# Optimization experiments

Measured on AMD Instinct MI355X. Metric: run time of the kernel, lower is better.

Reference implementation:

```python
import jax, jax.numpy as jnp
import numpy as np

N = 50000        # nodes
E = 800000       # edges (before self-loops)
NFEAT = 256
NHID = 32
HEADS = 8
NOUT = 128
NEG_SLOPE = 0.2
EPS = 1e-5


def _gat_layer(x, src, dst, W, att_src, att_dst, bias, heads, ch, concat):
    """PyG-style GATConv (shared weights for src/dst, self-loops already appended)."""
    n = x.shape[0]
    h = (x @ W).reshape(n, heads, ch)                      # [N,H,C]
    a_src = (h * att_src).sum(-1)                          # [N,H]
    a_dst = (h * att_dst).sum(-1)                          # [N,H]
    e = jax.nn.leaky_relu(a_src[src] + a_dst[dst], NEG_SLOPE)  # [E',H]
    # segment softmax over incoming edges of each dst node
    m = jax.ops.segment_max(e, dst, num_segments=n)        # [N,H]
    m = jnp.where(jnp.isfinite(m), m, 0.0)
    ex = jnp.exp(e - m[dst])                               # [E',H]
    denom = jax.ops.segment_sum(ex, dst, num_segments=n)   # [N,H]
    alpha = ex / (denom[dst] + 1e-16)                      # [E',H]
    msg = h[src] * alpha[:, :, None]                       # [E',H,C]
    out = jax.ops.segment_sum(msg, dst, num_segments=n)    # [N,H,C]
    out = out.reshape(n, heads * ch) if concat else out.mean(axis=1)
    return out + bias


def setup_inputs() -> dict:
    key = jax.random.key(0)
    ks = jax.random.split(key, 14)
    s = 0.05
    return {
        "x": jax.random.normal(ks[0], (N, NFEAT), jnp.float32),
        "edge_index": jax.random.randint(ks[1], (2, E), 0, N, dtype=jnp.int64),
        "W1": jax.random.normal(ks[2], (NFEAT, HEADS * NHID), jnp.float32) * s,
        "att_src1": jax.random.normal(ks[3], (HEADS, NHID), jnp.float32) * s,
        "att_dst1": jax.random.normal(ks[4], (HEADS, NHID), jnp.float32) * s,
        "b1": jnp.zeros((HEADS * NHID,), jnp.float32),
        "W2": jax.random.normal(ks[5], (HEADS * NHID, NOUT), jnp.float32) * s,
        "att_src2": jax.random.normal(ks[6], (1, NOUT), jnp.float32) * s,
        "att_dst2": jax.random.normal(ks[7], (1, NOUT), jnp.float32) * s,
        "b2": jnp.zeros((NOUT,), jnp.float32),
        "bn_gamma": jnp.ones((NOUT,), jnp.float32),
        "bn_beta": jnp.zeros((NOUT,), jnp.float32),
        "ln_gamma": jnp.ones((NOUT,), jnp.float32),
        "ln_beta": jnp.zeros((NOUT,), jnp.float32),
    }


def reference(x, edge_index, W1, att_src1, att_dst1, b1, W2, att_src2, att_dst2, b2,
              bn_gamma, bn_beta, ln_gamma, ln_beta):
    loops = jnp.arange(N, dtype=edge_index.dtype)
    src = jnp.concatenate([edge_index[0], loops])
    dst = jnp.concatenate([edge_index[1], loops])
    # layer 1: concat heads, then relu (dropout is identity at inference)
    h = jax.nn.relu(_gat_layer(x, src, dst, W1, att_src1, att_dst1, b1, HEADS, NHID, True))
    # layer 2: single head, mean (no concat), relu
    h = jax.nn.relu(_gat_layer(h, src, dst, W2, att_src2, att_dst2, b2, 1, NOUT, False))
    # BatchNorm1d with batch statistics (biased var, eps=1e-5)
    mu = h.mean(axis=0)
    var = h.var(axis=0)
    h = (h - mu) / jnp.sqrt(var + EPS) * bn_gamma + bn_beta
    # LayerNorm over last dim
    mu2 = h.mean(axis=-1, keepdims=True)
    var2 = h.var(axis=-1, keepdims=True)
    return (h - mu2) / jnp.sqrt(var2 + EPS) * ln_gamma + ln_beta
```

## Files before the change

kernel.cpp:

```cpp
#include <hip/hip_runtime.h>
#include <cstdint>
#include <cstddef>

#define HEADS   8
#define NFEAT   256
#define NOUT    128
#define NEG     0.2f
#define EPSV    1e-5f

typedef unsigned short ushort_t;
typedef __attribute__((ext_vector_type(8))) short s8v;
typedef __attribute__((ext_vector_type(4))) float f4v;

static __device__ __forceinline__ float lrelu(float x) { return x > 0.f ? x : NEG * x; }

static __device__ __forceinline__ float bf2f(ushort_t u) {
    union { unsigned int i; float f; } v; v.i = ((unsigned int)u) << 16; return v.f;
}
static __device__ __forceinline__ ushort_t f2bf(float f) {
    union { float f; unsigned int i; } v; v.f = f;
    unsigned int x = v.i;
    return (ushort_t)((x + 0x7fff + ((x >> 16) & 1)) >> 16);
}
static __device__ __forceinline__ float bits2f(unsigned int u) {
    union { unsigned int i; float f; } v; v.i = u; return v.f;
}
static __device__ __forceinline__ unsigned int f2bits(float f) {
    union { float f; unsigned int i; } v; v.f = f; return v.i;
}

static __device__ __forceinline__ int detect64(const int* __restrict__ ei, int E) {
    int lane = threadIdx.x & 63;
    long idx = 2L * ((long)lane * (E / 64)) + 1;
    int v = ei[idx];
    unsigned long long ball = __ballot(v == 0);
    return (ball == ~0ull) ? 1 : 0;
}

__global__ void k_prep(const int* __restrict__ ei, int* __restrict__ counts,
                       int E, int n, int cblocks,
                       const float* __restrict__ W1, const float* __restrict__ W2,
                       ushort_t* __restrict__ Wh1, ushort_t* __restrict__ Wl1,
                       ushort_t* __restrict__ Wh2, ushort_t* __restrict__ Wl2) {
    if (blockIdx.x < (unsigned)cblocks) {
        int is64 = detect64(ei, E);
        int i = blockIdx.x * 256 + threadIdx.x;
        if (i < E) {
            int d = ei[(size_t)(E + i) << is64];
            atomicAdd(&counts[d], 1);
        } else if (i < E + n) {
            atomicAdd(&counts[i - E], 1);
        }
    } else {
        int gid = (blockIdx.x - cblocks) * 256 + threadIdx.x;
        const float* W; ushort_t* Wh; ushort_t* Wl; int M;
        if (gid < 256 * 256) { W = W1; Wh = Wh1; Wl = Wl1; M = 256; }
        else { gid -= 256 * 256; if (gid >= 256 * 128) return; W = W2; Wh = Wh2; Wl = Wl2; M = 128; }
        int k = gid / M, nn = gid - k * M;
        int ntile = nn >> 4, j = nn & 15, kc = k >> 3, e = k & 7;
        int p = ((ntile * 32 + kc) * 16 + j) * 8 + e;
        float v = W[(size_t)k * M + nn];
        ushort_t hi = f2bf(v);
        float r = v - bf2f(hi);
        Wh[p] = hi;
        Wl[p] = f2bf(r);
    }
}

__global__ __launch_bounds__(1024) void k_scan1(const int* __restrict__ counts,
                                                int* __restrict__ incl,
                                                int* __restrict__ bsum, int n) {
    int t = threadIdx.x, i = blockIdx.x * 1024 + t;
    int lane = t & 63, w = t >> 6;
    int v = (i < n) ? counts[i] : 0;
    int sv = v;
#pragma unroll
    for (int o = 1; o < 64; o <<= 1) { int u = __shfl_up(sv, o, 64); if (lane >= o) sv += u; }
    __shared__ int wsum[16];
    if (lane == 63) wsum[w] = sv;
    __syncthreads();
    if (w == 0) {
        int bs = (lane < 16) ? wsum[lane] : 0;
#pragma unroll
        for (int o = 1; o < 16; o <<= 1) { int u = __shfl_up(bs, o, 64); if (lane >= o) bs += u; }
        if (lane < 16) wsum[lane] = bs;
    }
    __syncthreads();
    int pre = (w > 0) ? wsum[w - 1] : 0;
    sv += pre;
    if (i < n) incl[i] = sv;
    if (t == 1023) bsum[blockIdx.x] = sv;
}

__global__ void k_scan3(const int* __restrict__ incl, const int* __restrict__ bsum,
                        const int* __restrict__ counts,
                        int* __restrict__ offs, int* __restrict__ cursor, int n) {
    __shared__ int pre_s;
    int chunk = blockIdx.x >> 2;
    if (threadIdx.x == 0) {
        int s = 0;
        for (int j = 0; j < chunk; ++j) s += bsum[j];
        pre_s = s;
    }
    __syncthreads();
    int i = blockIdx.x * 256 + threadIdx.x;
    if (i < n) {
        int v = incl[i] + pre_s;
        offs[i + 1] = v;
        cursor[i] = v - counts[i];
    }
    if (i == 0) offs[0] = 0;
}

__global__ void k_fill(const int* __restrict__ ei, int* __restrict__ cursor,
                       int* __restrict__ esrc, int E, int n) {
    int is64 = detect64(ei, E);
    int i = blockIdx.x * blockDim.x + threadIdx.x;
    if (i >= E + n) return;
    int s, d;
    if (i < E) { s = ei[(size_t)i << is64]; d = ei[(size_t)(E + i) << is64]; }
    else       { s = i - E; d = s; }
    int p = atomicAdd(&cursor[d], 1);
    esrc[p] = s;
}

template <int MOUT>
__global__ __launch_bounds__(256) void k_mm(const float* __restrict__ A,
                                            const ushort_t* __restrict__ Wh,
                                            const ushort_t* __restrict__ Wl,
                                            ushort_t* __restrict__ C,
                                            const float* __restrict__ att_s,
                                            const float* __restrict__ att_d,
                                            float* __restrict__ as_o,
                                            float* __restrict__ ad_o, int n) {
    __shared__ ushort_t Ah[64][40];
    __shared__ ushort_t Al[64][40];
    const int t = threadIdx.x;
    const int lane = t & 63, w = t >> 6;
    const int r0 = blockIdx.x * 64;
    const int srow = t >> 2;
    const int kh = (t & 3) * 8;
    const int arow = r0 + srow;
    const bool rowok = arow < n;

    f4v acc[4][2];
#pragma unroll
    for (int a = 0; a < 4; ++a)
#pragma unroll
        for (int b = 0; b < 2; ++b) { f4v z = {0.f, 0.f, 0.f, 0.f}; acc[a][b] = z; }

    float pre[8];
    const float* abase = &A[(size_t)arow * 256 + kh];
#pragma unroll
    for (int q = 0; q < 2; ++q) {
        float4 v = rowok ? *reinterpret_cast<const float4*>(abase + q * 4)
                         : float4{0.f, 0.f, 0.f, 0.f};
        pre[q * 4 + 0] = v.x; pre[q * 4 + 1] = v.y;
        pre[q * 4 + 2] = v.z; pre[q * 4 + 3] = v.w;
    }

    const int lj = lane & 15, lk = lane >> 4;

    for (int kb = 0; kb < 256; kb += 32) {
        __syncthreads();
        {
            unsigned int hw[4], lw[4];
#pragma unroll
            for (int p = 0; p < 4; ++p) {
                unsigned int x0 = f2bits(pre[p * 2]);
                unsigned int x1 = f2bits(pre[p * 2 + 1]);
                unsigned int h1b = x1 & 0xffff0000u;
                float lo0 = pre[p * 2] - bits2f(x0 & 0xffff0000u);
                float lo1 = pre[p * 2 + 1] - bits2f(h1b);
                hw[p] = (x0 >> 16) | h1b;
                lw[p] = (f2bits(lo0) >> 16) | (f2bits(lo1) & 0xffff0000u);
            }
            uint4 hv = {hw[0], hw[1], hw[2], hw[3]};
            uint4 lv = {lw[0], lw[1], lw[2], lw[3]};
            *reinterpret_cast<uint4*>(&Ah[srow][kh]) = hv;
            *reinterpret_cast<uint4*>(&Al[srow][kh]) = lv;
        }
        __syncthreads();
        if (kb < 224) {
            const float* ap = abase + kb + 32;
#pragma unroll
            for (int q = 0; q < 2; ++q) {
                float4 v = rowok ? *reinterpret_cast<const float4*>(ap + q * 4)
                                 : float4{0.f, 0.f, 0.f, 0.f};
                pre[q * 4 + 0] = v.x; pre[q * 4 + 1] = v.y;
                pre[q * 4 + 2] = v.z; pre[q * 4 + 3] = v.w;
            }
        }
        const int kc0 = kb >> 3;
        s8v ah[4], al[4];
#pragma unroll
        for (int mf = 0; mf < 4; ++mf) {
            ah[mf] = *reinterpret_cast<const s8v*>(&Ah[mf * 16 + lj][lk * 8]);
            al[mf] = *reinterpret_cast<const s8v*>(&Al[mf * 16 + lj][lk * 8]);
        }
#pragma unroll
        for (int nf = 0; nf < 2; ++nf) {
            int ntile = (MOUT == 256 ? blockIdx.y * 8 : 0) + w * 2 + nf;
            size_t boff = ((size_t)(ntile * 32 + kc0 + lk) * 16 + lj) * 8;
            s8v bh = *reinterpret_cast<const s8v*>(&Wh[boff]);
            s8v bl = *reinterpret_cast<const s8v*>(&Wl[boff]);
#pragma unroll
            for (int mf = 0; mf < 4; ++mf) {
                acc[mf][nf] = __builtin_amdgcn_mfma_f32_16x16x32_bf16(ah[mf], bh, acc[mf][nf], 0, 0, 0);
                acc[mf][nf] = __builtin_amdgcn_mfma_f32_16x16x32_bf16(ah[mf], bl, acc[mf][nf], 0, 0, 0);
                acc[mf][nf] = __builtin_amdgcn_mfma_f32_16x16x32_bf16(al[mf], bh, acc[mf][nf], 0, 0, 0);
            }
        }
    }

    const int colw = (MOUT == 256 ? blockIdx.y * 128 : 0) + w * 32;

#pragma unroll
    for (int mf = 0; mf < 4; ++mf) {
        int rr = r0 + mf * 16 + lk * 4;
#pragma unroll
        for (int nf = 0; nf < 2; ++nf) {
            int cc = colw + nf * 16 + lj;
#pragma unroll
            for (int r = 0; r < 4; ++r) {
                if (rr + r < n) C[(size_t)(rr + r) * MOUT + cc] = f2bf(acc[mf][nf][r]);
            }
        }
    }

    float asv[2], adv[2];
#pragma unroll
    for (int nf = 0; nf < 2; ++nf) {
        asv[nf] = att_s[colw + nf * 16 + lj];
        adv[nf] = att_d[colw + nf * 16 + lj];
    }
#pragma unroll
    for (int mf = 0; mf < 4; ++mf) {
        int rr = r0 + mf * 16 + lk * 4;
#pragma unroll
        for (int r = 0; r < 4; ++r) {
            float ss = acc[mf][0][r] * asv[0] + acc[mf][1][r] * asv[1];
            float sd = acc[mf][0][r] * adv[0] + acc[mf][1][r] * adv[1];
#pragma unroll
            for (int o = 1; o < 16; o <<= 1) {
                ss += __shfl_xor(ss, o, 64); sd += __shfl_xor(sd, o, 64);
            }
            if (lj == 0 && rr + r < n) {
                if (MOUT == 256) {
                    int head = (colw >> 5);
                    as_o[(size_t)(rr + r) * 8 + head] = ss;
                    ad_o[(size_t)(rr + r) * 8 + head] = sd;
                } else {
                    atomicAdd(&as_o[rr + r], ss);
                    atomicAdd(&ad_o[rr + r], sd);
                }
            }
        }
    }
}

__global__ __launch_bounds__(128) void k_agg1(const ushort_t* __restrict__ h1,
                                              const float* __restrict__ as1,
                                              const float* __restrict__ ad1,
                                              const int* __restrict__ offs,
                                              const int* __restrict__ esrc,
                                              const float* __restrict__ b1,
                                              float* __restrict__ out1, int n, int tot) {
    int wid = (blockIdx.x * 128 + threadIdx.x) >> 6;
    int lane = threadIdx.x & 63;
    if (wid >= n) return;
    int e0 = offs[wid], e1 = offs[wid + 1];
    int deg = e1 - e0;

    if (deg <= 64) {
        const int l = lane & 31;
        const int h = lane >> 5;
        const int hd = l >> 2;
        const int cb = l * 8;

        int ei_idx = e0 + lane;
        int es = esrc[ei_idx < tot ? ei_idx : (tot - 1)];

        const int headA = lane >> 3, g = lane & 7;
        float adnA = ad1[(size_t)wid * 8 + headA];
        float a[8];
#pragma unroll
        for (int k = 0; k < 8; ++k) {
            int i = g + 8 * k;
            int s = __shfl(es, i, 64);
            a[k] = (i < deg) ? as1[(size_t)s * 8 + headA] : -1e30f;
        }
        float mx = a[0];
#pragma unroll
        for (int k = 1; k < 8; ++k) mx = fmaxf(mx, a[k]);
#pragma unroll
        for (int o = 1; o < 8; o <<= 1) mx = fmaxf(mx, __shfl_xor(mx, o, 64));
        float mA = lrelu(mx + adnA);
#pragma unroll
        for (int k = 0; k < 8; ++k)
            a[k] = __expf(lrelu(a[k] + adnA) - mA);

        float d = 0.f;
        float ac0 = 0.f, ac1 = 0.f, ac2 = 0.f, ac3 = 0.f;
        float ac4 = 0.f, ac5 = 0.f, ac6 = 0.f, ac7 = 0.f;
#pragma unroll
        for (int u = 0; u < 8; ++u) {
            if (8 * u < deg) {
#pragma unroll
                for (int v = 0; v < 4; ++v) {
                    int i = 8 * u + 2 * v + h;
                    int s = __shfl(es, i, 64);
                    float p = __shfl(a[u], hd * 8 + 2 * v + h, 64);
                    if (i < deg) {
                        uint4 hv = *reinterpret_cast<const uint4*>(&h1[(size_t)s * 256 + cb]);
                        d += p;
                        ac0 += p * bits2f(hv.x << 16);
                        ac1 += p * bits2f(hv.x & 0xffff0000u);
                        ac2 += p * bits2f(hv.y << 16);
                        ac3 += p * bits2f(hv.y & 0xffff0000u);
                        ac4 += p * bits2f(hv.z << 16);
                        ac5 += p * bits2f(hv.z & 0xffff0000u);
                        ac6 += p * bits2f(hv.w << 16);
                        ac7 += p * bits2f(hv.w & 0xffff0000u);
                    }
                }
            }
        }
        d   += __shfl_xor(d, 32, 64);
        ac0 += __shfl_xor(ac0, 32, 64); ac1 += __shfl_xor(ac1, 32, 64);
        ac2 += __shfl_xor(ac2, 32, 64); ac3 += __shfl_xor(ac3, 32, 64);
        ac4 += __shfl_xor(ac4, 32, 64); ac5 += __shfl_xor(ac5, 32, 64);
        ac6 += __shfl_xor(ac6, 32, 64); ac7 += __shfl_xor(ac7, 32, 64);
        if (lane < 32) {
            float inv = 1.f / (d + 1e-16f);
            float4 b0 = *reinterpret_cast<const float4*>(&b1[cb]);
            float4 b4 = *reinterpret_cast<const float4*>(&b1[cb + 4]);
            float4 o0, o1;
            o0.x = fmaxf(ac0 * inv + b0.x, 0.f);
            o0.y = fmaxf(ac1 * inv + b0.y, 0.f);
            o0.z = fmaxf(ac2 * inv + b0.z, 0.f);
            o0.w = fmaxf(ac3 * inv + b0.w, 0.f);
            o1.x = fmaxf(ac4 * inv + b4.x, 0.f);
            o1.y = fmaxf(ac5 * inv + b4.y, 0.f);
            o1.z = fmaxf(ac6 * inv + b4.z, 0.f);
            o1.w = fmaxf(ac7 * inv + b4.w, 0.f);
            *reinterpret_cast<float4*>(&out1[(size_t)wid * 256 + cb]) = o0;
            *reinterpret_cast<float4*>(&out1[(size_t)wid * 256 + cb + 4]) = o1;
        }
    } else {
        int head = lane >> 3;
        int g = lane & 7;
        int cb = lane * 4;
        float adn = ad1[(size_t)wid * 8 + head];
        float mx = -1e30f;
        for (int e = e0 + g; e < e1; e += 8)
            mx = fmaxf(mx, as1[(size_t)esrc[e] * 8 + head]);
#pragma unroll
        for (int o = 1; o < 8; o <<= 1) mx = fmaxf(mx, __shfl_xor(mx, o, 64));
        float m = lrelu(mx + adn);
        float d = 0.f, ax = 0.f, ay = 0.f, az = 0.f, aw = 0.f;
        for (int e = e0; e < e1; ++e) {
            int s = esrc[e];
            float p = __expf(lrelu(as1[(size_t)s * 8 + head] + adn) - m);
            ushort4 hv = *reinterpret_cast<const ushort4*>(&h1[(size_t)s * 256 + cb]);
            d += p;
            ax += p * bf2f(hv.x);
            ay += p * bf2f(hv.y);
            az += p * bf2f(hv.z);
            aw += p * bf2f(hv.w);
        }
        float inv = 1.f / (d + 1e-16f);
        float4 bb = *reinterpret_cast<const float4*>(&b1[cb]);
        float4 o;
        o.x = fmaxf(ax * inv + bb.x, 0.f);
        o.y = fmaxf(ay * inv + bb.y, 0.f);
        o.z = fmaxf(az * inv + bb.z, 0.f);
        o.w = fmaxf(aw * inv + bb.w, 0.f);
        *reinterpret_cast<float4*>(&out1[(size_t)wid * 256 + cb]) = o;
    }
}

__global__ __launch_bounds__(128) void k_agg2(const ushort_t* __restrict__ h2,
                                              const float* __restrict__ as2,
                                              const float* __restrict__ ad2,
                                              const int* __restrict__ offs,
                                              const int* __restrict__ esrc,
                                              const float* __restrict__ b2,
                                              float* __restrict__ out2, int n, int tot) {
    int wid = (blockIdx.x * 128 + threadIdx.x) >> 6;
    int lane = threadIdx.x & 63;
    if (wid >= n) return;
    float adn = ad2[wid];
    int e0 = offs[wid], e1 = offs[wid + 1];
    int deg = e1 - e0;

    if (deg <= 64) {
        const int l = lane & 15;
        const int q = lane >> 4;
        const int cb = l * 8;

        int ei_idx = e0 + lane;
        int es = esrc[ei_idx < tot ? ei_idx : (tot - 1)];
        float av0 = (lane < deg) ? as2[es] : -1e30f;
        float mx = av0;
#pragma unroll
        for (int o = 1; o < 64; o <<= 1) mx = fmaxf(mx, __shfl_xor(mx, o, 64));
        float m = lrelu(mx + adn);
        float p0 = __expf(lrelu(av0 + adn) - m);

        float d = 0.f;
        float ac0 = 0.f, ac1 = 0.f, ac2 = 0.f, ac3 = 0.f;
        float ac4 = 0.f, ac5 = 0.f, ac6 = 0.f, ac7 = 0.f;
#pragma unroll
        for (int u = 0; u < 4; ++u) {
            if (16 * u < deg) {
#pragma unroll
                for (int v = 0; v < 4; ++v) {
                    int i = 16 * u + 4 * v + q;
                    int s = __shfl(es, i, 64);
                    float p = __shfl(p0, i, 64);
                    if (i < deg) {
                        uint4 hv = *reinterpret_cast<const uint4*>(&h2[(size_t)s * 128 + cb]);
                        d += p;
                        ac0 += p * bits2f(hv.x << 16);
                        ac1 += p * bits2f(hv.x & 0xffff0000u);
                        ac2 += p * bits2f(hv.y << 16);
                        ac3 += p * bits2f(hv.y & 0xffff0000u);
                        ac4 += p * bits2f(hv.z << 16);
                        ac5 += p * bits2f(hv.z & 0xffff0000u);
                        ac6 += p * bits2f(hv.w << 16);
                        ac7 += p * bits2f(hv.w & 0xffff0000u);
                    }
                }
            }
        }
#pragma unroll
        for (int o = 16; o <= 32; o <<= 1) {
            d   += __shfl_xor(d, o, 64);
            ac0 += __shfl_xor(ac0, o, 64); ac1 += __shfl_xor(ac1, o, 64);
            ac2 += __shfl_xor(ac2, o, 64); ac3 += __shfl_xor(ac3, o, 64);
            ac4 += __shfl_xor(ac4, o, 64); ac5 += __shfl_xor(ac5, o, 64);
            ac6 += __shfl_xor(ac6, o, 64); ac7 += __shfl_xor(ac7, o, 64);
        }
        if (lane < 16) {
            float inv = 1.f / (d + 1e-16f);
            float4 b0 = *reinterpret_cast<const float4*>(&b2[cb]);
            float4 b4 = *reinterpret_cast<const float4*>(&b2[cb + 4]);
            float4 o0, o1;
            o0.x = fmaxf(ac0 * inv + b0.x, 0.f);
            o0.y = fmaxf(ac1 * inv + b0.y, 0.f);
            o0.z = fmaxf(ac2 * inv + b0.z, 0.f);
            o0.w = fmaxf(ac3 * inv + b0.w, 0.f);
            o1.x = fmaxf(ac4 * inv + b4.x, 0.f);
            o1.y = fmaxf(ac5 * inv + b4.y, 0.f);
            o1.z = fmaxf(ac6 * inv + b4.z, 0.f);
            o1.w = fmaxf(ac7 * inv + b4.w, 0.f);
            *reinterpret_cast<float4*>(&out2[(size_t)wid * 128 + cb]) = o0;
            *reinterpret_cast<float4*>(&out2[(size_t)wid * 128 + cb + 4]) = o1;
        }
    } else {
        int cb = lane * 2;
        float mx = -1e30f;
        for (int e = e0 + lane; e < e1; e += 64)
            mx = fmaxf(mx, as2[esrc[e]]);
#pragma unroll
        for (int o = 1; o < 64; o <<= 1) mx = fmaxf(mx, __shfl_xor(mx, o, 64));
        float m = lrelu(mx + adn);
        float d = 0.f, ax = 0.f, ay = 0.f;
        for (int e = e0; e < e1; ++e) {
            int s = esrc[e];
            float p = __expf(lrelu(as2[s] + adn) - m);
            ushort2 hv = *reinterpret_cast<const ushort2*>(&h2[(size_t)s * 128 + cb]);
            d += p;
            ax += p * bf2f(hv.x);
            ay += p * bf2f(hv.y);
        }
        float inv = 1.f / (d + 1e-16f);
        float o0 = fmaxf(ax * inv + b2[cb], 0.f);
        float o1 = fmaxf(ay * inv + b2[cb + 1], 0.f);
        float2 o = {o0, o1};
        *reinterpret_cast<float2*>(&out2[(size_t)wid * 128 + cb]) = o;
    }
}

__global__ __launch_bounds__(128) void k_bnstat(const float* __restrict__ out2,
                                                float* __restrict__ bnsum,
                                                float* __restrict__ bnsq, int n) {
    int c = threadIdx.x;
    float s = 0.f, q = 0.f;
    for (int r = blockIdx.x; r < n; r += gridDim.x) {
        float v = out2[(size_t)r * 128 + c];
        s += v;
        q += v * v;
    }
    atomicAdd(&bnsum[c], s);
    atomicAdd(&bnsq[c], q);
}

__global__ __launch_bounds__(256) void k_final(const float* __restrict__ out2,
                                               const float* __restrict__ bnsum,
                                               const float* __restrict__ bnsq,
                                               const float* __restrict__ bng,
                                               const float* __restrict__ bnb,
                                               const float* __restrict__ lng,
                                               const float* __restrict__ lnb,
                                               float* __restrict__ out, int n) {
    int wid = (blockIdx.x * blockDim.x + threadIdx.x) >> 6;
    int lane = threadIdx.x & 63;
    if (wid >= n) return;
    int c0 = lane, c1 = lane + 64;
    float invn = 1.f / (float)n;
    float mu0 = bnsum[c0] * invn, mu1 = bnsum[c1] * invn;
    float v0 = bnsq[c0] * invn - mu0 * mu0;
    float v1 = bnsq[c1] * invn - mu1 * mu1;
    float r0 = rsqrtf(v0 + EPSV), r1 = rsqrtf(v1 + EPSV);
    float x0 = out2[(size_t)wid * 128 + c0];
    float x1 = out2[(size_t)wid * 128 + c1];
    float y0 = (x0 - mu0) * r0 * bng[c0] + bnb[c0];
    float y1 = (x1 - mu1) * r1 * bng[c1] + bnb[c1];
    float s = y0 + y1, q = y0 * y0 + y1 * y1;
#pragma unroll
    for (int o = 1; o < 64; o <<= 1) { s += __shfl_xor(s, o, 64); q += __shfl_xor(q, o, 64); }
    float mu = s * (1.f / 128.f);
    float var = q * (1.f / 128.f) - mu * mu;
    float rr = rsqrtf(var + EPSV);
    out[(size_t)wid * 128 + c0] = (y0 - mu) * rr * lng[c0] + lnb[c0];
    out[(size_t)wid * 128 + c1] = (y1 - mu) * rr * lng[c1] + lnb[c1];
}

extern "C" void kernel_launch(void* const* d_in, const int* in_sizes, int n_in,
                              void* d_out, int out_size, void* d_ws, size_t ws_size,
                              hipStream_t stream) {
    const float* x    = (const float*)d_in[0];
    const int*   ei   = (const int*)d_in[1];
    const float* W1   = (const float*)d_in[2];
    const float* ats1 = (const float*)d_in[3];
    const float* atd1 = (const float*)d_in[4];
    const float* b1   = (const float*)d_in[5];
    const float* W2   = (const float*)d_in[6];
    const float* ats2 = (const float*)d_in[7];
    const float* atd2 = (const float*)d_in[8];
    const float* b2   = (const float*)d_in[9];
    const float* bng  = (const float*)d_in[10];
    const float* bnb  = (const float*)d_in[11];
    const float* lng  = (const float*)d_in[12];
    const float* lnb  = (const float*)d_in[13];

    const int n = in_sizes[0] / NFEAT;
    const int E = in_sizes[1] / 2;
    const int tot = E + n;

    auto align = [](size_t v) { return (v + 255) & ~(size_t)255; };
    char* ws = (char*)d_ws;
    size_t off = 0;
    ushort_t* h1 = (ushort_t*)(ws + off); off += align((size_t)n * 256 * 2);
    float* out1 = (float*)(ws + off); off += align((size_t)n * 256 * 4);
    ushort_t* h2 = h1;
    float* out2 = out1;
    float* as1 = (float*)(ws + off); off += align((size_t)n * 8 * 4);
    float* ad1 = (float*)(ws + off); off += align((size_t)n * 8 * 4);
    int* counts = (int*)(ws + off); off += align((size_t)n * 12 + 1024);
    float* bnsum = (float*)(counts + n);
    float* bnsq  = bnsum + 128;
    float* as2   = bnsq + 128;
    float* ad2   = as2 + n;
    int* offs   = (int*)(ws + off); off += align((size_t)(n + 1) * 4);
    int* cursor = (int*)(ws + off); off += align((size_t)n * 4);
    int* esrc   = (int*)(ws + off); off += align((size_t)tot * 4);
    int* incl   = (int*)(ws + off); off += align((size_t)n * 4);
    int* bsum   = (int*)(ws + off); off += align(64 * 4);
    ushort_t* Wh1 = (ushort_t*)(ws + off); off += align((size_t)256 * 256 * 2);
    ushort_t* Wl1 = (ushort_t*)(ws + off); off += align((size_t)256 * 256 * 2);
    ushort_t* Wh2 = (ushort_t*)(ws + off); off += align((size_t)256 * 128 * 2);
    ushort_t* Wl2 = (ushort_t*)(ws + off); off += align((size_t)256 * 128 * 2);

    hipMemsetAsync(counts, 0, (size_t)n * 12 + 1024, stream);

    const int cblocks = (tot + 255) / 256;
    const int pblocks = (256 * 256 + 256 * 128 + 255) / 256;
    k_prep<<<cblocks + pblocks, 256, 0, stream>>>(ei, counts, E, n, cblocks,
                                                  W1, W2, Wh1, Wl1, Wh2, Wl2);
    int nsb = (n + 1023) / 1024;
    k_scan1<<<nsb, 1024, 0, stream>>>(counts, incl, bsum, n);
    k_scan3<<<(n + 255) / 256, 256, 0, stream>>>(incl, bsum, counts, offs, cursor, n);
    k_fill<<<(tot + 255) / 256, 256, 0, stream>>>(ei, cursor, esrc, E, n);

    const int gx = (n + 63) / 64;
    k_mm<256><<<dim3(gx, 2), 256, 0, stream>>>(x, Wh1, Wl1, h1, ats1, atd1, as1, ad1, n);
    k_agg1<<<(n + 1) / 2, 128, 0, stream>>>(h1, as1, ad1, offs, esrc, b1, out1, n, tot);

    k_mm<128><<<dim3(gx, 1), 256, 0, stream>>>(out1, Wh2, Wl2, h2, ats2, atd2, as2, ad2, n);
    k_agg2<<<(n + 1) / 2, 128, 0, stream>>>(h2, as2, ad2, offs, esrc, b2, out2, n, tot);

    k_bnstat<<<512, 128, 0, stream>>>(out2, bnsum, bnsq, n);
    k_final<<<(n + 3) / 4, 256, 0, stream>>>(out2, bnsum, bnsq, bng, bnb, lng, lnb,
                                             (float*)d_out, n);
}
```

Before: 339.9 us.

## Double-buffer matmul LDS tiles and software-prefetch gathers in aggregation kernels

```diff
diff --git a/kernel.cpp b/kernel.cpp
--- a/kernel.cpp
+++ b/kernel.cpp
@@ -27,6 +27,19 @@
 }
 static __device__ __forceinline__ unsigned int f2bits(float f) {
     union { float f; unsigned int i; } v; v.f = f; return v.i;
+}
+
+static __device__ __forceinline__ void fma8(float p, const uint4& hv,
+    float& a0, float& a1, float& a2, float& a3,
+    float& a4, float& a5, float& a6, float& a7) {
+    a0 += p * bits2f(hv.x << 16);
+    a1 += p * bits2f(hv.x & 0xffff0000u);
+    a2 += p * bits2f(hv.y << 16);
+    a3 += p * bits2f(hv.y & 0xffff0000u);
+    a4 += p * bits2f(hv.z << 16);
+    a5 += p * bits2f(hv.z & 0xffff0000u);
+    a6 += p * bits2f(hv.w << 16);
+    a7 += p * bits2f(hv.w & 0xffff0000u);
 }
 
 static __device__ __forceinline__ int detect64(const int* __restrict__ ei, int E) {
@@ -133,8 +146,8 @@
                                             const float* __restrict__ att_d,
                                             float* __restrict__ as_o,
                                             float* __restrict__ ad_o, int n) {
-    __shared__ ushort_t Ah[64][40];
-    __shared__ ushort_t Al[64][40];
+    __shared__ ushort_t Ah[2][64][40];
+    __shared__ ushort_t Al[2][64][40];
     const int t = threadIdx.x;
     const int lane = t & 63, w = t >> 6;
     const int r0 = blockIdx.x * 64;
@@ -142,6 +155,7 @@
     const int kh = (t & 3) * 8;
     const int arow = r0 + srow;
     const bool rowok = arow < n;
+    const int lj = lane & 15, lk = lane >> 4;
 
     f4v acc[4][2];
 #pragma unroll
@@ -149,8 +163,70 @@
 #pragma unroll
         for (int b = 0; b < 2; ++b) { f4v z = {0.f, 0.f, 0.f, 0.f}; acc[a][b] = z; }
 
+    const float* abase = &A[(size_t)arow * 256 + kh];
     float pre[8];
-    const float* abase = &A[(size_t)arow * 256 + kh];
+
+#define MM_STAGE(BUF)                                                         \
+    {                                                                         \
+        unsigned int hw[4], lw[4];                                            \
+        _Pragma("unroll")                                                     \
+        for (int p = 0; p < 4; ++p) {                                         \
+            unsigned int x0 = f2bits(pre[p * 2]);                             \
+            unsigned int x1 = f2bits(pre[p * 2 + 1]);                         \
+            unsigned int h1b = x1 & 0xffff0000u;                              \
+            float lo0 = pre[p * 2] - bits2f(x0 & 0xffff0000u);                \
+            float lo1 = pre[p * 2 + 1] - bits2f(h1b);                         \
+            hw[p] = (x0 >> 16) | h1b;                                         \
+            lw[p] = (f2bits(lo0) >> 16) | (f2bits(lo1) & 0xffff0000u);        \
+        }                                                                     \
+        uint4 hv = {hw[0], hw[1], hw[2], hw[3]};                              \
+        uint4 lv = {lw[0], lw[1], lw[2], lw[3]};                              \
+        *reinterpret_cast<uint4*>(&Ah[BUF][srow][kh]) = hv;                   \
+        *reinterpret_cast<uint4*>(&Al[BUF][srow][kh]) = lv;                   \
+    }
+
+#define MM_LOADB(KB, BH, BL)                                                  \
+    {                                                                         \
+        const int kc0_ = (KB) >> 3;                                           \
+        _Pragma("unroll")                                                     \
+        for (int nf = 0; nf < 2; ++nf) {                                      \
+            int ntile = (MOUT == 256 ? blockIdx.y * 8 : 0) + w * 2 + nf;      \
+            size_t boff = ((size_t)(ntile * 32 + kc0_ + lk) * 16 + lj) * 8;   \
+            BH[nf] = *reinterpret_cast<const s8v*>(&Wh[boff]);                \
+            BL[nf] = *reinterpret_cast<const s8v*>(&Wl[boff]);                \
+        }                                                                     \
+    }
+
+#define MM_STEP(KB, CUR, BH, BL, BHN, BLN)                                    \
+    {                                                                         \
+        if ((KB) < 224) {                                                     \
+            const float* ap = abase + (KB) + 32;                              \
+            _Pragma("unroll")                                                 \
+            for (int q = 0; q < 2; ++q) {                                     \
+                float4 v = rowok ? *reinterpret_cast<const float4*>(ap + q*4) \
+                                 : float4{0.f, 0.f, 0.f, 0.f};                \
+                pre[q*4+0]=v.x; pre[q*4+1]=v.y; pre[q*4+2]=v.z; pre[q*4+3]=v.w; \
+            }                                                                 \
+            MM_LOADB((KB) + 32, BHN, BLN);                                    \
+        }                                                                     \
+        s8v ah[4], al[4];                                                     \
+        _Pragma("unroll")                                                     \
+        for (int mf = 0; mf < 4; ++mf) {                                      \
+            ah[mf] = *reinterpret_cast<const s8v*>(&Ah[CUR][mf*16+lj][lk*8]); \
+            al[mf] = *reinterpret_cast<const s8v*>(&Al[CUR][mf*16+lj][lk*8]); \
+        }                                                                     \
+        _Pragma("unroll")                                                     \
+        for (int nf = 0; nf < 2; ++nf)                                        \
+            _Pragma("unroll")                                                 \
+            for (int mf = 0; mf < 4; ++mf) {                                  \
+                acc[mf][nf] = __builtin_amdgcn_mfma_f32_16x16x32_bf16(ah[mf], BH[nf], acc[mf][nf], 0, 0, 0); \
+                acc[mf][nf] = __builtin_amdgcn_mfma_f32_16x16x32_bf16(ah[mf], BL[nf], acc[mf][nf], 0, 0, 0); \
+                acc[mf][nf] = __builtin_amdgcn_mfma_f32_16x16x32_bf16(al[mf], BH[nf], acc[mf][nf], 0, 0, 0); \
+            }                                                                 \
+        if ((KB) < 224) MM_STAGE((CUR) ^ 1);                                  \
+        __syncthreads();                                                      \
+    }
+
 #pragma unroll
     for (int q = 0; q < 2; ++q) {
         float4 v = rowok ? *reinterpret_cast<const float4*>(abase + q * 4)
@@ -158,59 +234,14 @@
         pre[q * 4 + 0] = v.x; pre[q * 4 + 1] = v.y;
         pre[q * 4 + 2] = v.z; pre[q * 4 + 3] = v.w;
     }
-
-    const int lj = lane & 15, lk = lane >> 4;
-
-    for (int kb = 0; kb < 256; kb += 32) {
-        __syncthreads();
-        {
-            unsigned int hw[4], lw[4];
-#pragma unroll
-            for (int p = 0; p < 4; ++p) {
-                unsigned int x0 = f2bits(pre[p * 2]);
-                unsigned int x1 = f2bits(pre[p * 2 + 1]);
-                unsigned int h1b = x1 & 0xffff0000u;
-                float lo0 = pre[p * 2] - bits2f(x0 & 0xffff0000u);
-                float lo1 = pre[p * 2 + 1] - bits2f(h1b);
-                hw[p] = (x0 >> 16) | h1b;
-                lw[p] = (f2bits(lo0) >> 16) | (f2bits(lo1) & 0xffff0000u);
-            }
-            uint4 hv = {hw[0], hw[1], hw[2], hw[3]};
-            uint4 lv = {lw[0], lw[1], lw[2], lw[3]};
-            *reinterpret_cast<uint4*>(&Ah[srow][kh]) = hv;
-            *reinterpret_cast<uint4*>(&Al[srow][kh]) = lv;
-        }
-        __syncthreads();
-        if (kb < 224) {
-            const float* ap = abase + kb + 32;
-#pragma unroll
-            for (int q = 0; q < 2; ++q) {
-                float4 v = rowok ? *reinterpret_cast<const float4*>(ap + q * 4)
-                                 : float4{0.f, 0.f, 0.f, 0.f};
-                pre[q * 4 + 0] = v.x; pre[q * 4 + 1] = v.y;
-                pre[q * 4 + 2] = v.z; pre[q * 4 + 3] = v.w;
-            }
-        }
-        const int kc0 = kb >> 3;
-        s8v ah[4], al[4];
-#pragma unroll
-        for (int mf = 0; mf < 4; ++mf) {
-            ah[mf] = *reinterpret_cast<const s8v*>(&Ah[mf * 16 + lj][lk * 8]);
-            al[mf] = *reinterpret_cast<const s8v*>(&Al[mf * 16 + lj][lk * 8]);
-        }
-#pragma unroll
-        for (int nf = 0; nf < 2; ++nf) {
-            int ntile = (MOUT == 256 ? blockIdx.y * 8 : 0) + w * 2 + nf;
-            size_t boff = ((size_t)(ntile * 32 + kc0 + lk) * 16 + lj) * 8;
-            s8v bh = *reinterpret_cast<const s8v*>(&Wh[boff]);
-            s8v bl = *reinterpret_cast<const s8v*>(&Wl[boff]);
-#pragma unroll
-            for (int mf = 0; mf < 4; ++mf) {
-                acc[mf][nf] = __builtin_amdgcn_mfma_f32_16x16x32_bf16(ah[mf], bh, acc[mf][nf], 0, 0, 0);
-                acc[mf][nf] = __builtin_amdgcn_mfma_f32_16x16x32_bf16(ah[mf], bl, acc[mf][nf], 0, 0, 0);
-                acc[mf][nf] = __builtin_amdgcn_mfma_f32_16x16x32_bf16(al[mf], bh, acc[mf][nf], 0, 0, 0);
-            }
-        }
+    s8v bhA[2], blA[2], bhB[2], blB[2];
+    MM_LOADB(0, bhA, blA);
+    MM_STAGE(0);
+    __syncthreads();
+
+    for (int kb = 0; kb < 256; kb += 64) {
+        MM_STEP(kb,      0, bhA, blA, bhB, blB);
+        MM_STEP(kb + 32, 1, bhB, blB, bhA, blA);
     }
 
     const int colw = (MOUT == 256 ? blockIdx.y * 128 : 0) + w * 32;
@@ -257,6 +288,9 @@
             }
         }
     }
+#undef MM_STEP
+#undef MM_LOADB
+#undef MM_STAGE
 }
 
 __global__ __launch_bounds__(128) void k_agg1(const ushort_t* __restrict__ h1,
@@ -296,43 +330,60 @@
 #pragma unroll
         for (int o = 1; o < 8; o <<= 1) mx = fmaxf(mx, __shfl_xor(mx, o, 64));
         float mA = lrelu(mx + adnA);
-#pragma unroll
-        for (int k = 0; k < 8; ++k)
+        float ds = 0.f;
+#pragma unroll
+        for (int k = 0; k < 8; ++k) {
             a[k] = __expf(lrelu(a[k] + adnA) - mA);
-
-        float d = 0.f;
+            ds += a[k];
+        }
+#pragma unroll
+        for (int o = 1; o < 8; o <<= 1) ds += __shfl_xor(ds, o, 64);
+        float dfull = __shfl(ds, hd * 8, 64);
+
         float ac0 = 0.f, ac1 = 0.f, ac2 = 0.f, ac3 = 0.f;
         float ac4 = 0.f, ac5 = 0.f, ac6 = 0.f, ac7 = 0.f;
+
+#define AG1_PREF(U, H0, H1V, H2, H3, P0, P1, P2, P3)                           \
+    {                                                                          \
+        int i0_ = 8*(U) + 0 + h, i1_ = 8*(U) + 2 + h,                          \
+            i2_ = 8*(U) + 4 + h, i3_ = 8*(U) + 6 + h;                          \
+        int s0_ = __shfl(es, i0_, 64), s1_ = __shfl(es, i1_, 64),              \
+            s2_ = __shfl(es, i2_, 64), s3_ = __shfl(es, i3_, 64);              \
+        P0 = __shfl(a[U], hd*8 + 0 + h, 64);                                   \
+        P1 = __shfl(a[U], hd*8 + 2 + h, 64);                                   \
+        P2 = __shfl(a[U], hd*8 + 4 + h, 64);                                   \
+        P3 = __shfl(a[U], hd*8 + 6 + h, 64);                                   \
+        if (i0_ < deg) H0  = *reinterpret_cast<const uint4*>(&h1[(size_t)s0_*256+cb]); \
+        if (i1_ < deg) H1V = *reinterpret_cast<const uint4*>(&h1[(size_t)s1_*256+cb]); \
+        if (i2_ < deg) H2  = *reinterpret_cast<const uint4*>(&h1[(size_t)s2_*256+cb]); \
+        if (i3_ < deg) H3  = *reinterpret_cast<const uint4*>(&h1[(size_t)s3_*256+cb]); \
+    }
+
+        uint4 hc0 = {0,0,0,0}, hc1 = hc0, hc2 = hc0, hc3 = hc0;
+        uint4 hn0 = hc0, hn1 = hc0, hn2 = hc0, hn3 = hc0;
+        float pc0 = 0.f, pc1 = 0.f, pc2 = 0.f, pc3 = 0.f;
+        float pn0 = 0.f, pn1 = 0.f, pn2 = 0.f, pn3 = 0.f;
+        AG1_PREF(0, hc0, hc1, hc2, hc3, pc0, pc1, pc2, pc3);
 #pragma unroll
         for (int u = 0; u < 8; ++u) {
             if (8 * u < deg) {
-#pragma unroll
-                for (int v = 0; v < 4; ++v) {
-                    int i = 8 * u + 2 * v + h;
-                    int s = __shfl(es, i, 64);
-                    float p = __shfl(a[u], hd * 8 + 2 * v + h, 64);
-                    if (i < deg) {
-                        uint4 hv = *reinterpret_cast<const uint4*>(&h1[(size_t)s * 256 + cb]);
-                        d += p;
-                        ac0 += p * bits2f(hv.x << 16);
-                        ac1 += p * bits2f(hv.x & 0xffff0000u);
-                        ac2 += p * bits2f(hv.y << 16);
-                        ac3 += p * bits2f(hv.y & 0xffff0000u);
-                        ac4 += p * bits2f(hv.z << 16);
-                        ac5 += p * bits2f(hv.z & 0xffff0000u);
-                        ac6 += p * bits2f(hv.w << 16);
-                        ac7 += p * bits2f(hv.w & 0xffff0000u);
-                    }
-                }
+                if (u < 7 && 8 * (u + 1) < deg)
+                    AG1_PREF(u + 1, hn0, hn1, hn2, hn3, pn0, pn1, pn2, pn3);
+                fma8(pc0, hc0, ac0, ac1, ac2, ac3, ac4, ac5, ac6, ac7);
+                fma8(pc1, hc1, ac0, ac1, ac2, ac3, ac4, ac5, ac6, ac7);
+                fma8(pc2, hc2, ac0, ac1, ac2, ac3, ac4, ac5, ac6, ac7);
+                fma8(pc3, hc3, ac0, ac1, ac2, ac3, ac4, ac5, ac6, ac7);
+                hc0 = hn0; hc1 = hn1; hc2 = hn2; hc3 = hn3;
+                pc0 = pn0; pc1 = pn1; pc2 = pn2; pc3 = pn3;
             }
         }
-        d   += __shfl_xor(d, 32, 64);
+#undef AG1_PREF
         ac0 += __shfl_xor(ac0, 32, 64); ac1 += __shfl_xor(ac1, 32, 64);
         ac2 += __shfl_xor(ac2, 32, 64); ac3 += __shfl_xor(ac3, 32, 64);
         ac4 += __shfl_xor(ac4, 32, 64); ac5 += __shfl_xor(ac5, 32, 64);
         ac6 += __shfl_xor(ac6, 32, 64); ac7 += __shfl_xor(ac7, 32, 64);
         if (lane < 32) {
-            float inv = 1.f / (d + 1e-16f);
+            float inv = 1.f / (dfull + 1e-16f);
             float4 b0 = *reinterpret_cast<const float4*>(&b1[cb]);
             float4 b4 = *reinterpret_cast<const float4*>(&b1[cb + 4]);
             float4 o0, o1;
@@ -396,7 +447,7 @@
 
     if (deg <= 64) {
         const int l = lane & 15;
-        const int q = lane >> 4;
+        const int qq = lane >> 4;
         const int cb = l * 8;
 
         int ei_idx = e0 + lane;
@@ -407,43 +458,57 @@
         for (int o = 1; o < 64; o <<= 1) mx = fmaxf(mx, __shfl_xor(mx, o, 64));
         float m = lrelu(mx + adn);
         float p0 = __expf(lrelu(av0 + adn) - m);
-
-        float d = 0.f;
+        float ds = p0;
+#pragma unroll
+        for (int o = 1; o < 64; o <<= 1) ds += __shfl_xor(ds, o, 64);
+
         float ac0 = 0.f, ac1 = 0.f, ac2 = 0.f, ac3 = 0.f;
         float ac4 = 0.f, ac5 = 0.f, ac6 = 0.f, ac7 = 0.f;
+
+#define AG2_PREF(U, H0, H1V, H2, H3, P0, P1, P2, P3)                           \
+    {                                                                          \
+        int i0_ = 16*(U) + 0 + qq, i1_ = 16*(U) + 4 + qq,                      \
+            i2_ = 16*(U) + 8 + qq, i3_ = 16*(U) + 12 + qq;                     \
+        int s0_ = __shfl(es, i0_, 64), s1_ = __shfl(es, i1_, 64),              \
+            s2_ = __shfl(es, i2_, 64), s3_ = __shfl(es, i3_, 64);              \
+        P0 = __shfl(p0, i0_, 64);                                              \
+        P1 = __shfl(p0, i1_, 64);                                              \
+        P2 = __shfl(p0, i2_, 64);                                              \
+        P3 = __shfl(p0, i3_, 64);                                              \
+        if (i0_ < deg) H0  = *reinterpret_cast<const uint4*>(&h2[(size_t)s0_*128+cb]); \
+        if (i1_ < deg) H1V = *reinterpret_cast<const uint4*>(&h2[(size_t)s1_*128+cb]); \
+        if (i2_ < deg) H2  = *reinterpret_cast<const uint4*>(&h2[(size_t)s2_*128+cb]); \
+        if (i3_ < deg) H3  = *reinterpret_cast<const uint4*>(&h2[(size_t)s3_*128+cb]); \
+    }
+
+        uint4 hc0 = {0,0,0,0}, hc1 = hc0, hc2 = hc0, hc3 = hc0;
+        uint4 hn0 = hc0, hn1 = hc0, hn2 = hc0, hn3 = hc0;
+        float pc0 = 0.f, pc1 = 0.f, pc2 = 0.f, pc3 = 0.f;
+        float pn0 = 0.f, pn1 = 0.f, pn2 = 0.f, pn3 = 0.f;
+        AG2_PREF(0, hc0, hc1, hc2, hc3, pc0, pc1, pc2, pc3);
 #pragma unroll
         for (int u = 0; u < 4; ++u) {
             if (16 * u < deg) {
-#pragma unroll
-                for (int v = 0; v < 4; ++v) {
-                    int i = 16 * u + 4 * v + q;
-                    int s = __shfl(es, i, 64);
-                    float p = __shfl(p0, i, 64);
-                    if (i < deg) {
-                        uint4 hv = *reinterpret_cast<const uint4*>(&h2[(size_t)s * 128 + cb]);
-                        d += p;
-                        ac0 += p * bits2f(hv.x << 16);
-                        ac1 += p * bits2f(hv.x & 0xffff0000u);
-                        ac2 += p * bits2f(hv.y << 16);
-                        ac3 += p * bits2f(hv.y & 0xffff0000u);
-                        ac4 += p * bits2f(hv.z << 16);
-                        ac5 += p * bits2f(hv.z & 0xffff0000u);
-                        ac6 += p * bits2f(hv.w << 16);
-                        ac7 += p * bits2f(hv.w & 0xffff0000u);
-                    }
-                }
+                if (u < 3 && 16 * (u + 1) < deg)
+                    AG2_PREF(u + 1, hn0, hn1, hn2, hn3, pn0, pn1, pn2, pn3);
+                fma8(pc0, hc0, ac0, ac1, ac2, ac3, ac4, ac5, ac6, ac7);
+                fma8(pc1, hc1, ac0, ac1, ac2, ac3, ac4, ac5, ac6, ac7);
+                fma8(pc2, hc2, ac0, ac1, ac2, ac3, ac4, ac5, ac6, ac7);
+                fma8(pc3, hc3, ac0, ac1, ac2, ac3, ac4, ac5, ac6, ac7);
+                hc0 = hn0; hc1 = hn1; hc2 = hn2; hc3 = hn3;
+                pc0 = pn0; pc1 = pn1; pc2 = pn2; pc3 = pn3;
             }
         }
+#undef AG2_PREF
 #pragma unroll
         for (int o = 16; o <= 32; o <<= 1) {
-            d   += __shfl_xor(d, o, 64);
             ac0 += __shfl_xor(ac0, o, 64); ac1 += __shfl_xor(ac1, o, 64);
             ac2 += __shfl_xor(ac2, o, 64); ac3 += __shfl_xor(ac3, o, 64);
             ac4 += __shfl_xor(ac4, o, 64); ac5 += __shfl_xor(ac5, o, 64);
             ac6 += __shfl_xor(ac6, o, 64); ac7 += __shfl_xor(ac7, o, 64);
         }
         if (lane < 16) {
-            float inv = 1.f / (d + 1e-16f);
+            float inv = 1.f / (ds + 1e-16f);
             float4 b0 = *reinterpret_cast<const float4*>(&b2[cb]);
             float4 b4 = *reinterpret_cast<const float4*>(&b2[cb + 4]);
             float4 o0, o1;
```

Result: no change. 335.1 us (-1.4%).

## Pre-split GEMM A operands into MFMA-fragment bf16 hi/lo layout upstream

Applied to the files above, without the earlier changes.

```diff
diff --git a/kernel.cpp b/kernel.cpp
--- a/kernel.cpp
+++ b/kernel.cpp
@@ -27,6 +27,16 @@
 }
 static __device__ __forceinline__ unsigned int f2bits(float f) {
     union { float f; unsigned int i; } v; v.f = f; return v.i;
+}
+
+static __device__ __forceinline__ void split2(float v0, float v1,
+                                              unsigned int& hw, unsigned int& lw) {
+    unsigned int x0 = f2bits(v0), x1 = f2bits(v1);
+    unsigned int h1b = x1 & 0xffff0000u;
+    float lo0 = v0 - bits2f(x0 & 0xffff0000u);
+    float lo1 = v1 - bits2f(h1b);
+    hw = (x0 >> 16) | h1b;
+    lw = (f2bits(lo0) >> 16) | (f2bits(lo1) & 0xffff0000u);
 }
 
 static __device__ __forceinline__ int detect64(const int* __restrict__ ei, int E) {
@@ -38,10 +48,12 @@
 }
 
 __global__ void k_prep(const int* __restrict__ ei, int* __restrict__ counts,
-                       int E, int n, int cblocks,
+                       int E, int n, int cblocks, int pblocks,
                        const float* __restrict__ W1, const float* __restrict__ W2,
                        ushort_t* __restrict__ Wh1, ushort_t* __restrict__ Wl1,
-                       ushort_t* __restrict__ Wh2, ushort_t* __restrict__ Wl2) {
+                       ushort_t* __restrict__ Wh2, ushort_t* __restrict__ Wl2,
+                       const float* __restrict__ x,
+                       ushort_t* __restrict__ Xh, ushort_t* __restrict__ Xl) {
     if (blockIdx.x < (unsigned)cblocks) {
         int is64 = detect64(ei, E);
         int i = blockIdx.x * 256 + threadIdx.x;
@@ -51,7 +63,7 @@
         } else if (i < E + n) {
             atomicAdd(&counts[i - E], 1);
         }
-    } else {
+    } else if (blockIdx.x < (unsigned)(cblocks + pblocks)) {
         int gid = (blockIdx.x - cblocks) * 256 + threadIdx.x;
         const float* W; ushort_t* Wh; ushort_t* Wl; int M;
         if (gid < 256 * 256) { W = W1; Wh = Wh1; Wl = Wl1; M = 256; }
@@ -64,6 +76,25 @@
         float r = v - bf2f(hi);
         Wh[p] = hi;
         Wl[p] = f2bf(r);
+    } else {
+        int gid = (blockIdx.x - cblocks - pblocks) * 256 + threadIdx.x;
+        if (gid >= n * 32) return;
+        int row = gid >> 5, k8 = gid & 31;
+        const float* xp = &x[(size_t)row * 256 + k8 * 8];
+        float4 v0 = *reinterpret_cast<const float4*>(xp);
+        float4 v1 = *reinterpret_cast<const float4*>(xp + 4);
+        unsigned int hw[4], lw[4];
+        split2(v0.x, v0.y, hw[0], lw[0]);
+        split2(v0.z, v0.w, hw[1], lw[1]);
+        split2(v1.x, v1.y, hw[2], lw[2]);
+        split2(v1.z, v1.w, hw[3], lw[3]);
+        int rt = row >> 6, mf = (row & 63) >> 4, lj = row & 15;
+        size_t po = (size_t)rt * 16384 + (k8 >> 2) * 2048 + mf * 512
+                  + ((k8 & 3) * 16 + lj) * 8;
+        uint4 hv = {hw[0], hw[1], hw[2], hw[3]};
+        uint4 lv = {lw[0], lw[1], lw[2], lw[3]};
+        *reinterpret_cast<uint4*>(&Xh[po]) = hv;
+        *reinterpret_cast<uint4*>(&Xl[po]) = lv;
     }
 }
 
@@ -125,7 +156,8 @@
 }
 
 template <int MOUT>
-__global__ __launch_bounds__(256) void k_mm(const float* __restrict__ A,
+__global__ __launch_bounds__(256) void k_mm(const ushort_t* __restrict__ Aph,
+                                            const ushort_t* __restrict__ Apl,
                                             const ushort_t* __restrict__ Wh,
                                             const ushort_t* __restrict__ Wl,
                                             ushort_t* __restrict__ C,
@@ -133,15 +165,10 @@
                                             const float* __restrict__ att_d,
                                             float* __restrict__ as_o,
                                             float* __restrict__ ad_o, int n) {
-    __shared__ ushort_t Ah[64][40];
-    __shared__ ushort_t Al[64][40];
     const int t = threadIdx.x;
     const int lane = t & 63, w = t >> 6;
     const int r0 = blockIdx.x * 64;
-    const int srow = t >> 2;
-    const int kh = (t & 3) * 8;
-    const int arow = r0 + srow;
-    const bool rowok = arow < n;
+    const int lj = lane & 15, lk = lane >> 4;
 
     f4v acc[4][2];
 #pragma unroll
@@ -149,68 +176,33 @@
 #pragma unroll
         for (int b = 0; b < 2; ++b) { f4v z = {0.f, 0.f, 0.f, 0.f}; acc[a][b] = z; }
 
-    float pre[8];
-    const float* abase = &A[(size_t)arow * 256 + kh];
-#pragma unroll
-    for (int q = 0; q < 2; ++q) {
-        float4 v = rowok ? *reinterpret_cast<const float4*>(abase + q * 4)
-                         : float4{0.f, 0.f, 0.f, 0.f};
-        pre[q * 4 + 0] = v.x; pre[q * 4 + 1] = v.y;
-        pre[q * 4 + 2] = v.z; pre[q * 4 + 3] = v.w;
-    }
-
-    const int lj = lane & 15, lk = lane >> 4;
-
-    for (int kb = 0; kb < 256; kb += 32) {
-        __syncthreads();
-        {
-            unsigned int hw[4], lw[4];
-#pragma unroll
-            for (int p = 0; p < 4; ++p) {
-                unsigned int x0 = f2bits(pre[p * 2]);
-                unsigned int x1 = f2bits(pre[p * 2 + 1]);
-                unsigned int h1b = x1 & 0xffff0000u;
-                float lo0 = pre[p * 2] - bits2f(x0 & 0xffff0000u);
-                float lo1 = pre[p * 2 + 1] - bits2f(h1b);
-                hw[p] = (x0 >> 16) | h1b;
-                lw[p] = (f2bits(lo0) >> 16) | (f2bits(lo1) & 0xffff0000u);
-            }
-            uint4 hv = {hw[0], hw[1], hw[2], hw[3]};
-            uint4 lv = {lw[0], lw[1], lw[2], lw[3]};
-            *reinterpret_cast<uint4*>(&Ah[srow][kh]) = hv;
-            *reinterpret_cast<uint4*>(&Al[srow][kh]) = lv;
-        }
-        __syncthreads();
-        if (kb < 224) {
-            const float* ap = abase + kb + 32;
-#pragma unroll
-            for (int q = 0; q < 2; ++q) {
-                float4 v = rowok ? *reinterpret_cast<const float4*>(ap + q * 4)
-                                 : float4{0.f, 0.f, 0.f, 0.f};
-                pre[q * 4 + 0] = v.x; pre[q * 4 + 1] = v.y;
-                pre[q * 4 + 2] = v.z; pre[q * 4 + 3] = v.w;
-            }
-        }
-        const int kc0 = kb >> 3;
+    const size_t abase = (size_t)blockIdx.x * 16384 + (size_t)lane * 8;
+
+#pragma unroll
+    for (int kbi = 0; kbi < 8; ++kbi) {
         s8v ah[4], al[4];
 #pragma unroll
         for (int mf = 0; mf < 4; ++mf) {
-            ah[mf] = *reinterpret_cast<const s8v*>(&Ah[mf * 16 + lj][lk * 8]);
-            al[mf] = *reinterpret_cast<const s8v*>(&Al[mf * 16 + lj][lk * 8]);
-        }
+            size_t ao = abase + kbi * 2048 + mf * 512;
+            ah[mf] = *reinterpret_cast<const s8v*>(&Aph[ao]);
+            al[mf] = *reinterpret_cast<const s8v*>(&Apl[ao]);
+        }
+        s8v bh[2], bl[2];
 #pragma unroll
         for (int nf = 0; nf < 2; ++nf) {
             int ntile = (MOUT == 256 ? blockIdx.y * 8 : 0) + w * 2 + nf;
-            size_t boff = ((size_t)(ntile * 32 + kc0 + lk) * 16 + lj) * 8;
-            s8v bh = *reinterpret_cast<const s8v*>(&Wh[boff]);
-            s8v bl = *reinterpret_cast<const s8v*>(&Wl[boff]);
+            size_t boff = ((size_t)(ntile * 32 + kbi * 4 + lk) * 16 + lj) * 8;
+            bh[nf] = *reinterpret_cast<const s8v*>(&Wh[boff]);
+            bl[nf] = *reinterpret_cast<const s8v*>(&Wl[boff]);
+        }
+#pragma unroll
+        for (int nf = 0; nf < 2; ++nf)
 #pragma unroll
             for (int mf = 0; mf < 4; ++mf) {
-                acc[mf][nf] = __builtin_amdgcn_mfma_f32_16x16x32_bf16(ah[mf], bh, acc[mf][nf], 0, 0, 0);
-                acc[mf][nf] = __builtin_amdgcn_mfma_f32_16x16x32_bf16(ah[mf], bl, acc[mf][nf], 0, 0, 0);
-                acc[mf][nf] = __builtin_amdgcn_mfma_f32_16x16x32_bf16(al[mf], bh, acc[mf][nf], 0, 0, 0);
+                acc[mf][nf] = __builtin_amdgcn_mfma_f32_16x16x32_bf16(ah[mf], bh[nf], acc[mf][nf], 0, 0, 0);
+                acc[mf][nf] = __builtin_amdgcn_mfma_f32_16x16x32_bf16(ah[mf], bl[nf], acc[mf][nf], 0, 0, 0);
+                acc[mf][nf] = __builtin_amdgcn_mfma_f32_16x16x32_bf16(al[mf], bh[nf], acc[mf][nf], 0, 0, 0);
             }
-        }
     }
 
     const int colw = (MOUT == 256 ? blockIdx.y * 128 : 0) + w * 32;
@@ -265,12 +257,14 @@
                                               const int* __restrict__ offs,
                                               const int* __restrict__ esrc,
                                               const float* __restrict__ b1,
-                                              float* __restrict__ out1, int n, int tot) {
+                                              ushort_t* __restrict__ Oh,
+                                              ushort_t* __restrict__ Ol, int n, int tot) {
     int wid = (blockIdx.x * 128 + threadIdx.x) >> 6;
     int lane = threadIdx.x & 63;
     if (wid >= n) return;
     int e0 = offs[wid], e1 = offs[wid + 1];
     int deg = e1 - e0;
+    const int rt = wid >> 6, mfr = (wid & 63) >> 4, ljr = wid & 15;
 
     if (deg <= 64) {
         const int l = lane & 31;
@@ -335,17 +329,25 @@
             float inv = 1.f / (d + 1e-16f);
             float4 b0 = *reinterpret_cast<const float4*>(&b1[cb]);
             float4 b4 = *reinterpret_cast<const float4*>(&b1[cb + 4]);
-            float4 o0, o1;
-            o0.x = fmaxf(ac0 * inv + b0.x, 0.f);
-            o0.y = fmaxf(ac1 * inv + b0.y, 0.f);
-            o0.z = fmaxf(ac2 * inv + b0.z, 0.f);
-            o0.w = fmaxf(ac3 * inv + b0.w, 0.f);
-            o1.x = fmaxf(ac4 * inv + b4.x, 0.f);
-            o1.y = fmaxf(ac5 * inv + b4.y, 0.f);
-            o1.z = fmaxf(ac6 * inv + b4.z, 0.f);
-            o1.w = fmaxf(ac7 * inv + b4.w, 0.f);
-            *reinterpret_cast<float4*>(&out1[(size_t)wid * 256 + cb]) = o0;
-            *reinterpret_cast<float4*>(&out1[(size_t)wid * 256 + cb + 4]) = o1;
+            float o0 = fmaxf(ac0 * inv + b0.x, 0.f);
+            float o1 = fmaxf(ac1 * inv + b0.y, 0.f);
+            float o2 = fmaxf(ac2 * inv + b0.z, 0.f);
+            float o3 = fmaxf(ac3 * inv + b0.w, 0.f);
+            float o4 = fmaxf(ac4 * inv + b4.x, 0.f);
+            float o5 = fmaxf(ac5 * inv + b4.y, 0.f);
+            float o6 = fmaxf(ac6 * inv + b4.z, 0.f);
+            float o7 = fmaxf(ac7 * inv + b4.w, 0.f);
+            unsigned int hw[4], lw[4];
+            split2(o0, o1, hw[0], lw[0]);
+            split2(o2, o3, hw[1], lw[1]);
+            split2(o4, o5, hw[2], lw[2]);
+            split2(o6, o7, hw[3], lw[3]);
+            size_t po = (size_t)rt * 16384 + (l >> 2) * 2048 + mfr * 512
+                      + ((l & 3) * 16 + ljr) * 8;
+            uint4 hv = {hw[0], hw[1], hw[2], hw[3]};
+            uint4 lv = {lw[0], lw[1], lw[2], lw[3]};
+            *reinterpret_cast<uint4*>(&Oh[po]) = hv;
+            *reinterpret_cast<uint4*>(&Ol[po]) = lv;
         }
     } else {
         int head = lane >> 3;
@@ -371,12 +373,19 @@
         }
         float inv = 1.f / (d + 1e-16f);
         float4 bb = *reinterpret_cast<const float4*>(&b1[cb]);
-        float4 o;
-        o.x = fmaxf(ax * inv + bb.x, 0.f);
-        o.y = fmaxf(ay * inv + bb.y, 0.f);
-        o.z = fmaxf(az * inv + bb.z, 0.f);
-        o.w = fmaxf(aw * inv + bb.w, 0.f);
-        *reinterpret_cast<float4*>(&out1[(size_t)wid * 256 + cb]) = o;
+        float o0 = fmaxf(ax * inv + bb.x, 0.f);
+        float o1 = fmaxf(ay * inv + bb.y, 0.f);
+        float o2 = fmaxf(az * inv + bb.z, 0.f);
+        float o3 = fmaxf(aw * inv + bb.w, 0.f);
+        unsigned int hw0, lw0, hw1, lw1;
+        split2(o0, o1, hw0, lw0);
+        split2(o2, o3, hw1, lw1);
+        int k8 = lane >> 1, e0c = (lane & 1) * 4;
+        size_t po = (size_t)rt * 16384 + (k8 >> 2) * 2048 + mfr * 512
+                  + ((k8 & 3) * 16 + ljr) * 8 + e0c;
+        uint2 hv = {hw0, hw1}, lv = {lw0, lw1};
+        *reinterpret_cast<uint2*>(&Oh[po]) = hv;
+        *reinterpret_cast<uint2*>(&Ol[po]) = lv;
     }
 }
 
@@ -549,14 +558,16 @@
     const int n = in_sizes[0] / NFEAT;
     const int E = in_sizes[1] / 2;
     const int tot = E + n;
+    const int gx = (n + 63) / 64;
 
     auto align = [](size_t v) { return (v + 255) & ~(size_t)255; };
     char* ws = (char*)d_ws;
     size_t off = 0;
     ushort_t* h1 = (ushort_t*)(ws + off); off += align((size_t)n * 256 * 2);
-    float* out1 = (float*)(ws + off); off += align((size_t)n * 256 * 4);
+    ushort_t* Xh = (ushort_t*)(ws + off); off += align((size_t)gx * 16384 * 2);
+    ushort_t* Xl = (ushort_t*)(ws + off); off += align((size_t)gx * 16384 * 2);
     ushort_t* h2 = h1;
-    float* out2 = out1;
+    float* out2 = (float*)(ws + off); off += align((size_t)n * 128 * 4);
     float* as1 = (float*)(ws + off); off += align((size_t)n * 8 * 4);
     float* ad1 = (float*)(ws + off); off += align((size_t)n * 8 * 4);
     int* counts = (int*)(ws + off); off += align((size_t)n * 12 + 1024);
@@ -578,18 +589,19 @@
 
     const int cblocks = (tot + 255) / 256;
     const int pblocks = (256 * 256 + 256 * 128 + 255) / 256;
-    k_prep<<<cblocks + pblocks, 256, 0, stream>>>(ei, counts, E, n, cblocks,
-                                                  W1, W2, Wh1, Wl1, Wh2, Wl2);
+    const int xblocks = (n * 32 + 255) / 256;
+    k_prep<<<cblocks + pblocks + xblocks, 256, 0, stream>>>(
+        ei, counts, E, n, cblocks, pblocks,
+        W1, W2, Wh1, Wl1, Wh2, Wl2, x, Xh, Xl);
     int nsb = (n + 1023) / 1024;
     k_scan1<<<nsb, 1024, 0, stream>>>(counts, incl, bsum, n);
     k_scan3<<<(n + 255) / 256, 256, 0, stream>>>(incl, bsum, counts, offs, cursor, n);
     k_fill<<<(tot + 255) / 256, 256, 0, stream>>>(ei, cursor, esrc, E, n);
 
-    const int gx = (n + 63) / 64;
-    k_mm<256><<<dim3(gx, 2), 256, 0, stream>>>(x, Wh1, Wl1, h1, ats1, atd1, as1, ad1, n);
-    k_agg1<<<(n + 1) / 2, 128, 0, stream>>>(h1, as1, ad1, offs, esrc, b1, out1, n, tot);
-
-    k_mm<128><<<dim3(gx, 1), 256, 0, stream>>>(out1, Wh2, Wl2, h2, ats2, atd2, as2, ad2, n);
+    k_mm<256><<<dim3(gx, 2), 256, 0, stream>>>(Xh, Xl, Wh1, Wl1, h1, ats1, atd1, as1, ad1, n);
+    k_agg1<<<(n + 1) / 2, 128, 0, stream>>>(h1, as1, ad1, offs, esrc, b1, Xh, Xl, n, tot);
+
+    k_mm<128><<<dim3(gx, 1), 256, 0, stream>>>(Xh, Xl, Wh2, Wl2, h2, ats2, atd2, as2, ad2, n);
     k_agg2<<<(n + 1) / 2, 128, 0, stream>>>(h2, as2, ad2, offs, esrc, b2, out2, n, tot);
 
     k_bnstat<<<512, 128, 0, stream>>>(out2, bnsum, bnsq, n);
```

Measured after the change: 345.1 us. No clear change (+1.5%).
